# Kernel optimization log

Measured on AMD Instinct MI355X. Metric: run time of the kernel, lower is better.

The kernel has to match this reference:

```python
import jax, jax.numpy as jnp
import numpy as np

N, S, E, H = 8, 1024, 1024, 16
DK = E // H

def setup_inputs() -> dict:
    key = jax.random.key(0)
    ks = jax.random.split(key, 10)
    s = 1.0 / np.sqrt(E)
    x = jax.random.normal(ks[0], (N, S, E), dtype=jnp.float32)
    attn_mask = jax.random.randint(ks[1], (N, S, S), 0, 2) == 1
    Wq = jax.random.normal(ks[2], (E, E), dtype=jnp.float32) * s
    Wk = jax.random.normal(ks[3], (E, E), dtype=jnp.float32) * s
    Wv = jax.random.normal(ks[4], (E, E), dtype=jnp.float32) * s
    Wo = jax.random.normal(ks[5], (E, E), dtype=jnp.float32) * s
    bq = jax.random.normal(ks[6], (E,), dtype=jnp.float32) * s
    bk = jax.random.normal(ks[7], (E,), dtype=jnp.float32) * s
    bv = jax.random.normal(ks[8], (E,), dtype=jnp.float32) * s
    bo = jax.random.normal(ks[9], (E,), dtype=jnp.float32) * s
    return {"x": x, "attn_mask": attn_mask, "Wq": Wq, "bq": bq, "Wk": Wk, "bk": bk,
            "Wv": Wv, "bv": bv, "Wo": Wo, "bo": bo}

def reference(x, attn_mask, Wq, bq, Wk, bk, Wv, bv, Wo, bo):
    n, s, e = x.shape
    # projections, split into heads: (N, H, S, DK)
    q = (x @ Wq + bq).reshape(n, s, H, DK).transpose(0, 2, 1, 3)
    k = (x @ Wk + bk).reshape(n, s, H, DK).transpose(0, 2, 1, 3)
    v = (x @ Wv + bv).reshape(n, s, H, DK).transpose(0, 2, 1, 3)
    logits = jnp.einsum("nhqd,nhkd->nhqk", q, k) / np.sqrt(DK).astype(np.float32)
    # mask==True positions are suppressed (masked_fill with -1e9)
    logits = jnp.where(attn_mask[:, None, :, :], jnp.float32(-1e9), logits)
    attn = jax.nn.softmax(logits, axis=-1)  # exp(log_softmax) == softmax
    o = jnp.einsum("nhqk,nhkd->nhqd", attn, v)
    o = o.transpose(0, 2, 1, 3).reshape(n, s, e)
    return o @ Wo + bo
```

## Files before the change

kernel.cpp:

```cpp
#include <hip/hip_runtime.h>
#include <hip/hip_bf16.h>

typedef unsigned short u16;
typedef unsigned int   u32;
typedef unsigned long long u64;

#define SEQ 1024
#define EMB 1024
#define NH  16
#define DKH 64

#define QSCALE 0.18033688f

typedef __attribute__((ext_vector_type(8))) short short8;
typedef __attribute__((ext_vector_type(4))) float floatx4;

__device__ __forceinline__ float b2f(u16 u) {
  return __uint_as_float(((u32)u) << 16);
}
__device__ __forceinline__ u16 f2b(float f) {
  u32 u = __float_as_uint(f);
  u32 r = u + 0x7fffu + ((u >> 16) & 1u);
  return (u16)(r >> 16);
}

__device__ __forceinline__ void glds16(const u16* g, u16* l) {
  __builtin_amdgcn_global_load_lds(
      (const __attribute__((address_space(1))) u32*)g,
      (__attribute__((address_space(3))) u32*)l, 16, 0, 0);
}

__global__ __launch_bounds__(256) void probe_inputs(const u32* __restrict__ A,
                                                    const u32* __restrict__ B,
                                                    int* __restrict__ flags) {
  __shared__ int mA, mB, mBig, xB16;
  if (threadIdx.x == 0) { mA = 0; mB = 0; mBig = 0; xB16 = 0; }
  __syncthreads();
  int la = 0, lb = 0;
  for (int i = threadIdx.x; i < 4096; i += 256) {
    if ((A[i] & 0xFEFEFEFEu) == 0) la++;
    if ((B[i] & 0xFEFEFEFEu) == 0) lb++;
  }
  atomicAdd(&mA, la); atomicAdd(&mB, lb);
  __syncthreads();
  const int xIsB = (mA > mB) ? 1 : 0;
  const u32* X = xIsB ? B : A;
  const u32* M = xIsB ? A : B;
  int big = 0, cnt = 0;
  for (int i = threadIdx.x; i < 4096; i += 256)
    if (M[i] > 1u) big = 1;
  for (int i = threadIdx.x; i < 2048; i += 256) {
    u16 v = (u16)(X[i] & 0xffffu);
    int e = (v >> 7) & 0xFF;
    if (e >= 110 && e <= 135) cnt++;
  }
  if (big) atomicOr(&mBig, 1);
  atomicAdd(&xB16, cnt);
  __syncthreads();
  if (threadIdx.x == 0) {
    flags[0] = xIsB;
    flags[1] = (xB16 > 1500) ? 1 : 0;
    flags[2] = mBig;
  }
}

__global__ __launch_bounds__(256) void preprocess(
    const void* __restrict__ bigA, const void* __restrict__ bigB,
    const int* __restrict__ flags,
    u16* __restrict__ xb, u32* __restrict__ maskbits,
    const void* __restrict__ w0, const void* __restrict__ w1,
    const void* __restrict__ w2, const void* __restrict__ w3,
    u16* __restrict__ outQKV, u16* __restrict__ outO,
    const void* __restrict__ b0, const void* __restrict__ b1,
    const void* __restrict__ b2, const void* __restrict__ b3,
    float* __restrict__ biasf) {
  __shared__ float tile[32][33];
  const int bidg = blockIdx.x;
  const int t = threadIdx.x;
  const int amode = flags[1];

  if (bidg < 8192) {
    const void* x = flags[0] ? bigB : bigA;
    int i = (bidg * 256 + t) * 4;
    if (amode) {
      *(ushort4*)(xb + i) = *(const ushort4*)((const u16*)x + i);
    } else {
      float4 v = *(const float4*)((const float*)x + i);
      ushort4 o;
      o.x = f2b(v.x); o.y = f2b(v.y); o.z = f2b(v.z); o.w = f2b(v.w);
      *(ushort4*)(xb + i) = o;
    }
  } else if (bidg < 9216) {
    const void* mask = flags[0] ? bigA : bigB;
    const int mbyte = flags[2];
    const int lane = t & 63, wv = t >> 6;
    const u64 base0 = (u64)(bidg - 8192) * 8192;
#pragma unroll 4
    for (int k = 0; k < 32; k++) {
      u64 idx = base0 + k * 256 + t;
      int v;
      if (mbyte) v = ((const unsigned char*)mask)[idx] == 0;
      else       v = ((const u32*)mask)[idx] == 0;
      u64 b = __ballot(v);
      if (lane == 0) {
        u64 wbase = (base0 + k * 256 + wv * 64) >> 5;
        maskbits[wbase]     = (u32)b;
        maskbits[wbase + 1] = (u32)(b >> 32);
      }
    }
  } else if (bidg < 13312) {
    const int idx = bidg - 9216;
    const int z = idx >> 10;
    const int byi = (idx & 1023) >> 5;
    const int bxi = idx & 31;
    const void* in = (z == 0) ? w0 : (z == 1) ? w1 : (z == 2) ? w2 : w3;
    u16* out = (z < 3) ? (outQKV + (u64)z * EMB * EMB) : outO;
    const float scale = (z == 0) ? QSCALE : 1.0f;
    const int tx = t & 31;
    const int ty = t >> 5;
    const int bx = bxi * 32, by = byi * 32;
    if (amode) {
      const u16* inb = (const u16*)in;
#pragma unroll
      for (int r = ty; r < 32; r += 8)
        tile[r][tx] = b2f(inb[(u64)(by + r) * EMB + bx + tx]);
    } else {
      const float* inf = (const float*)in;
#pragma unroll
      for (int r = ty; r < 32; r += 8)
        tile[r][tx] = inf[(u64)(by + r) * EMB + bx + tx];
    }
    __syncthreads();
#pragma unroll
    for (int r = ty; r < 32; r += 8)
      out[(u64)(bx + r) * EMB + by + tx] = f2b(tile[tx][r] * scale);
  } else {
    const int widx = bidg - 13312;
    const void* ptrs[4] = {b0, b1, b2, b3};
    const void* p = ptrs[widx];
    const float scale = (widx == 0) ? QSCALE : 1.0f;
    for (int i = t; i < 1024; i += 256) {
      float v = amode ? b2f(((const u16*)p)[i]) : ((const float*)p)[i];
      biasf[widx * 1024 + i] = v * scale;
    }
  }
}


template <int OUTMODE>
__device__ __forceinline__ void gemm_core(
    const u16* __restrict__ X, const u16* __restrict__ Wt,
    const float* __restrict__ bias,
    u16* __restrict__ Qg, u16* __restrict__ Kg, u16* __restrict__ Vt,
    float* __restrict__ outf, int row0) {
  __shared__ __align__(16) u16 lds[2][(256 + 128) * 64];
  const int t = threadIdx.x;
  const int lane = t & 63;
  const int w = t >> 6;
  const int wr = w >> 1, wc = w & 1;
  const int l15 = lane & 15, l4 = lane >> 4;

  const int nwg = gridDim.x * gridDim.y;
  const int bid0 = blockIdx.y * gridDim.x + blockIdx.x;
  const int cpx = nwg >> 3;
  const int swz = (bid0 & 7) * cpx + (bid0 >> 3);
  const int bM = (swz % gridDim.x) * 256;
  const int bN = (swz / gridDim.x) * 128;

  const int r7 = l15 & 7;
  const int cA = (l4 ^ r7) << 3;
  const int cB = (l4 ^ r7 ^ 4) << 3;

  floatx4 acc[4][4];
#pragma unroll
  for (int i = 0; i < 4; i++)
#pragma unroll
    for (int j = 0; j < 4; j++)
      acc[i][j] = (floatx4){0.f, 0.f, 0.f, 0.f};

  const int srow = w * 8 + (lane >> 3);
  const int schk = ((lane & 7) ^ (lane >> 3)) << 3;
  const u16* Ap = X + (u64)(row0 + bM + srow) * EMB + schk;
  const u16* Bp = Wt + (u64)(bN + srow) * EMB + schk;
  u16* Ad0 = &lds[0][w * 512];
  u16* Bd0 = &lds[0][16384 + w * 512];
  u16* Ad1 = &lds[1][w * 512];
  u16* Bd1 = &lds[1][16384 + w * 512];

  auto stage = [&](u16* Ad, u16* Bd, int k0) {
    glds16(Ap + k0, Ad);
    glds16(Ap + k0 + 64 * EMB, Ad + 4096);
    glds16(Ap + k0 + 128 * EMB, Ad + 8192);
    glds16(Ap + k0 + 192 * EMB, Ad + 12288);
    glds16(Bp + k0, Bd);
    glds16(Bp + k0 + 64 * EMB, Bd + 4096);
  };

  auto compute = [&](const u16* __restrict__ Ab, const u16* __restrict__ Bb) {
    short8 af[2][2], bfr[4][2];
#pragma unroll
    for (int n = 0; n < 4; n++) {
      const int gr = (wc * 64 + n * 16 + l15) * 64;
      bfr[n][0] = *(const short8*)(&Bb[gr + cA]);
      bfr[n][1] = *(const short8*)(&Bb[gr + cB]);
    }
#pragma unroll
    for (int mh = 0; mh < 2; mh++) {
      short8 af2[2][2];
#pragma unroll
      for (int m = 0; m < 2; m++) {
        const int fr = (wr * 64 + mh * 32 + m * 16 + l15) * 64;
        af2[m][0] = *(const short8*)(&Ab[fr + cA]);
        af2[m][1] = *(const short8*)(&Ab[fr + cB]);
      }
      __builtin_amdgcn_s_setprio(1);
#pragma unroll
      for (int m = 0; m < 2; m++)
#pragma unroll
        for (int n = 0; n < 4; n++) {
          acc[mh * 2 + m][n] = __builtin_amdgcn_mfma_f32_16x16x32_bf16(
              af2[m][0], bfr[n][0], acc[mh * 2 + m][n], 0, 0, 0);
          acc[mh * 2 + m][n] = __builtin_amdgcn_mfma_f32_16x16x32_bf16(
              af2[m][1], bfr[n][1], acc[mh * 2 + m][n], 0, 0, 0);
        }
      __builtin_amdgcn_s_setprio(0);
      (void)af[0][0];
    }
  };

  stage(Ad0, Bd0, 0);
  for (int k0 = 0; k0 < EMB; k0 += 128) {
    stage(Ad1, Bd1, k0 + 64);
    asm volatile("s_waitcnt vmcnt(6)" ::: "memory");
    asm volatile("s_barrier" ::: "memory");
    compute(&lds[0][0], &lds[0][16384]);
    asm volatile("s_barrier" ::: "memory");
    if (k0 + 128 < EMB) {
      stage(Ad0, Bd0, k0 + 128);
      asm volatile("s_waitcnt vmcnt(6)" ::: "memory");
    } else {
      asm volatile("s_waitcnt vmcnt(0)" ::: "memory");
    }
    asm volatile("s_barrier" ::: "memory");
    compute(&lds[1][0], &lds[1][16384]);
    asm volatile("s_barrier" ::: "memory");
  }

  if (OUTMODE == 0) {
    const int sec = bN >> 10;
    if (sec < 2) {
      u16* outp = (sec == 0) ? Qg : Kg;
#pragma unroll
      for (int n = 0; n < 4; n++) {
        int col = bN + wc * 64 + n * 16 + l15;
        float bv = bias[col];
        int colh = col & 1023;
        int h = colh >> 6, d = colh & 63;
#pragma unroll
        for (int mt = 0; mt < 4; mt++) {
#pragma unroll
          for (int r = 0; r < 4; r++) {
            int row = bM + wr * 64 + mt * 16 + l4 * 4 + r;
            float v = acc[mt][n][r] + bv;
            int nb = row >> 10, s = row & 1023;
            outp[((u64)((nb * NH + h) * SEQ + s)) * DKH + d] = f2b(v);
          }
        }
      }
    } else {
      u16* ldt = &lds[0][0];
#pragma unroll
      for (int n = 0; n < 4; n++) {
        const int dl = wc * 64 + n * 16 + l15;
        const float bv = bias[bN + dl];
#pragma unroll
        for (int mt = 0; mt < 4; mt++) {
          const int sb = wr * 64 + mt * 16 + l4 * 4;
          const int sp = sb ^ ((dl & 7) << 3);
          u32 w0 = (u32)f2b(acc[mt][n][0] + bv) |
                   ((u32)f2b(acc[mt][n][1] + bv) << 16);
          u32 w1 = (u32)f2b(acc[mt][n][2] + bv) |
                   ((u32)f2b(acc[mt][n][3] + bv) << 16);
          *(u32*)(&ldt[dl * 256 + sp])     = w0;
          *(u32*)(&ldt[dl * 256 + sp + 2]) = w1;
        }
      }
      __syncthreads();
      const int d  = t >> 2;
      const int sq = (t & 3) * 64;
      const int arow = row0 + bM;
      const int nb = arow >> 10, s0 = arow & 1023;
      const int h = ((bN & 1023) >> 6) + (d >> 6);
      u16* vout = Vt + (u64)(nb * NH + h) * SEQ * DKH +
                  (u64)(d & 63) * SEQ + s0 + sq;
#pragma unroll
      for (int c = 0; c < 8; c++) {
        const int sc = sq + c * 8;
        const int scs = sc ^ ((d & 7) << 3);
        *(uint4*)(vout + c * 8) = *(const uint4*)(&ldt[d * 256 + scs]);
      }
    }
  } else {
#pragma unroll
    for (int n = 0; n < 4; n++) {
      int col = bN + wc * 64 + n * 16 + l15;
      float bv = bias[col];
#pragma unroll
      for (int mt = 0; mt < 4; mt++) {
#pragma unroll
        for (int r = 0; r < 4; r++) {
          int row = bM + wr * 64 + mt * 16 + l4 * 4 + r;
          outf[(u64)row * EMB + col] = acc[mt][n][r] + bv;
        }
      }
    }
  }
}

__global__ __launch_bounds__(512, 2) void gemm_qkv(
    const u16* __restrict__ X, const u16* __restrict__ Wt,
    const float* __restrict__ bias,
    u16* __restrict__ Qg, u16* __restrict__ Kg, u16* __restrict__ Vt,
    int row0) {
  gemm_core<0>(X, Wt, bias, Qg, Kg, Vt, nullptr, row0);
}

__global__ __launch_bounds__(512, 2) void gemm_out(
    const u16* __restrict__ X, const u16* __restrict__ Wt,
    const float* __restrict__ bias, float* __restrict__ out) {
  gemm_core<1>(X, Wt, bias, nullptr, nullptr, nullptr, out, 0);
}

__global__ __launch_bounds__(512, 4) void attn_mfma(
    const u16* __restrict__ Q, const u16* __restrict__ K,
    const u16* __restrict__ Vt, const u32* __restrict__ maskbits,
    int b0, u16* __restrict__ ctx) {
  __shared__ __align__(16) u16 Ks[2][64 * 64];
  __shared__ __align__(16) u16 Vs[64 * 64];
  __shared__ __align__(16) u16 Ps[256 * 64];

  const int t = threadIdx.x;
  const int lane = t & 63, w = t >> 6;
  const int l15 = lane & 15, l4 = lane >> 4;
  const int bid = blockIdx.x;
  const int h = bid & 15;
  const int qt = (bid >> 4) & 3;
  const int n = bid >> 6;
  const int nh = n * NH + h;
  const int q0 = qt * 256;
  const u64 hoff = (u64)nh * SEQ * DKH;

  const int r7 = l15 & 7;
  const int cA = (l4 ^ r7) << 3;
  const int cB = (l4 ^ r7 ^ 4) << 3;

  const int rt = w * 8 + (lane >> 3);
  const int chk = ((lane & 7) ^ (lane >> 3)) << 3;
  const u16* Kp = K + hoff + (u64)rt * DKH + chk;
  const u16* Vp = Vt + hoff + (u64)rt * SEQ + chk;
  const int ldsO = w * 512;

  short8 qf[2][2];
  {
    const u16* qpA = Q + hoff + (u64)(q0 + w * 32 + l15) * DKH + l4 * 8;
    qf[0][0] = *(const short8*)(qpA);
    qf[0][1] = *(const short8*)(qpA + 32);
    const u16* qpB = qpA + 16 * DKH;
    qf[1][0] = *(const short8*)(qpB);
    qf[1][1] = *(const short8*)(qpB + 32);
  }

  short8 ones;
#pragma unroll
  for (int e = 0; e < 8; e++) ones[e] = (short)0x3F80;

  floatx4 o[2][4];
#pragma unroll
  for (int s = 0; s < 2; s++)
#pragma unroll
    for (int j = 0; j < 4; j++) o[s][j] = (floatx4){0.f, 0.f, 0.f, 0.f};
  floatx4 osum[2];
  osum[0] = (floatx4){0.f, 0.f, 0.f, 0.f};
  osum[1] = (floatx4){0.f, 0.f, 0.f, 0.f};

  const u64 mrow0 = ((u64)((b0 + n) * SEQ + q0 + w * 32 + l15)) * 32;
  const u64 mrow1 = mrow0 + 16 * 32;
  const int pq0 = w * 32 + l15;
  const int pq1 = pq0 + 16;
  const int pc0 = (l4 * 4) ^ (r7 << 3);

  glds16(Kp, &Ks[0][ldsO]);
  glds16(Vp, &Vs[ldsO]);
  __syncthreads();

  int cur = 0;
  for (int kc = 0; kc < SEQ; kc += 64) {
    if (kc > 0) glds16(Vp + kc, &Vs[ldsO]);
    const int havek = (kc + 64 < SEQ);
    if (havek) glds16(Kp + (kc + 64) * DKH, &Ks[cur ^ 1][ldsO]);

    const u64 mb0 = *(const u64*)(maskbits + mrow0 + (kc >> 5));
    const u64 mb1 = *(const u64*)(maskbits + mrow1 + (kc >> 5));
    const u16* Kc = &Ks[cur][0];

    __builtin_amdgcn_s_setprio(1);
#pragma unroll
    for (int j = 0; j < 4; j++) {
      const int rb = (j * 16 + l15) * 64;
      short8 kb0 = *(const short8*)(&Kc[rb + cA]);
      short8 kb1 = *(const short8*)(&Kc[rb + cB]);
      floatx4 s0 = (floatx4){0.f, 0.f, 0.f, 0.f};
      floatx4 s1 = (floatx4){0.f, 0.f, 0.f, 0.f};
      s0 = __builtin_amdgcn_mfma_f32_16x16x32_bf16(kb0, qf[0][0], s0, 0, 0, 0);
      s0 = __builtin_amdgcn_mfma_f32_16x16x32_bf16(kb1, qf[0][1], s0, 0, 0, 0);
      s1 = __builtin_amdgcn_mfma_f32_16x16x32_bf16(kb0, qf[1][0], s1, 0, 0, 0);
      s1 = __builtin_amdgcn_mfma_f32_16x16x32_bf16(kb1, qf[1][1], s1, 0, 0, 0);

      const u32 mj0 = (u32)(mb0 >> (j * 16 + l4 * 4));
      const u32 mj1 = (u32)(mb1 >> (j * 16 + l4 * 4));
      float p00 = __uint_as_float(
          __float_as_uint(__builtin_amdgcn_exp2f(s0[0])) &
          (u32)__builtin_amdgcn_sbfe(mj0, 0, 1));
      float p01 = __uint_as_float(
          __float_as_uint(__builtin_amdgcn_exp2f(s0[1])) &
          (u32)__builtin_amdgcn_sbfe(mj0, 1, 1));
      float p02 = __uint_as_float(
          __float_as_uint(__builtin_amdgcn_exp2f(s0[2])) &
          (u32)__builtin_amdgcn_sbfe(mj0, 2, 1));
      float p03 = __uint_as_float(
          __float_as_uint(__builtin_amdgcn_exp2f(s0[3])) &
          (u32)__builtin_amdgcn_sbfe(mj0, 3, 1));
      float p10 = __uint_as_float(
          __float_as_uint(__builtin_amdgcn_exp2f(s1[0])) &
          (u32)__builtin_amdgcn_sbfe(mj1, 0, 1));
      float p11 = __uint_as_float(
          __float_as_uint(__builtin_amdgcn_exp2f(s1[1])) &
          (u32)__builtin_amdgcn_sbfe(mj1, 1, 1));
      float p12 = __uint_as_float(
          __float_as_uint(__builtin_amdgcn_exp2f(s1[2])) &
          (u32)__builtin_amdgcn_sbfe(mj1, 2, 1));
      float p13 = __uint_as_float(
          __float_as_uint(__builtin_amdgcn_exp2f(s1[3])) &
          (u32)__builtin_amdgcn_sbfe(mj1, 3, 1));

      uint2 pk0, pk1;
      asm("v_cvt_pk_bf16_f32 %0, %1, %2" : "=v"(pk0.x) : "v"(p00), "v"(p01));
      asm("v_cvt_pk_bf16_f32 %0, %1, %2" : "=v"(pk0.y) : "v"(p02), "v"(p03));
      asm("v_cvt_pk_bf16_f32 %0, %1, %2" : "=v"(pk1.x) : "v"(p10), "v"(p11));
      asm("v_cvt_pk_bf16_f32 %0, %1, %2" : "=v"(pk1.y) : "v"(p12), "v"(p13));
      const int pcol = (j * 16) ^ pc0;
      *(uint2*)(&Ps[pq0 * 64 + pcol]) = pk0;
      *(uint2*)(&Ps[pq1 * 64 + pcol]) = pk1;
    }

    if (havek) asm volatile("s_waitcnt vmcnt(1)" ::: "memory");
    else       asm volatile("s_waitcnt vmcnt(0)" ::: "memory");
    __builtin_amdgcn_s_barrier();

    short8 pa[2][2];
    pa[0][0] = *(const short8*)(&Ps[pq0 * 64 + cA]);
    pa[0][1] = *(const short8*)(&Ps[pq0 * 64 + cB]);
    pa[1][0] = *(const short8*)(&Ps[pq1 * 64 + cA]);
    pa[1][1] = *(const short8*)(&Ps[pq1 * 64 + cB]);
#pragma unroll
    for (int j = 0; j < 4; j++) {
      const int rb = (j * 16 + l15) * 64;
      short8 vb0 = *(const short8*)(&Vs[rb + cA]);
      short8 vb1 = *(const short8*)(&Vs[rb + cB]);
      o[0][j] = __builtin_amdgcn_mfma_f32_16x16x32_bf16(pa[0][0], vb0, o[0][j], 0, 0, 0);
      o[0][j] = __builtin_amdgcn_mfma_f32_16x16x32_bf16(pa[0][1], vb1, o[0][j], 0, 0, 0);
      o[1][j] = __builtin_amdgcn_mfma_f32_16x16x32_bf16(pa[1][0], vb0, o[1][j], 0, 0, 0);
      o[1][j] = __builtin_amdgcn_mfma_f32_16x16x32_bf16(pa[1][1], vb1, o[1][j], 0, 0, 0);
    }
    osum[0] = __builtin_amdgcn_mfma_f32_16x16x32_bf16(pa[0][0], ones, osum[0], 0, 0, 0);
    osum[0] = __builtin_amdgcn_mfma_f32_16x16x32_bf16(pa[0][1], ones, osum[0], 0, 0, 0);
    osum[1] = __builtin_amdgcn_mfma_f32_16x16x32_bf16(pa[1][0], ones, osum[1], 0, 0, 0);
    osum[1] = __builtin_amdgcn_mfma_f32_16x16x32_bf16(pa[1][1], ones, osum[1], 0, 0, 0);
    __builtin_amdgcn_s_setprio(0);

    __syncthreads();
    cur ^= 1;
  }

#pragma unroll
  for (int s = 0; s < 2; s++) {
#pragma unroll
    for (int r = 0; r < 4; r++) {
      float invr = 1.0f / fmaxf(osum[s][r], 1e-30f);
      int q = q0 + w * 32 + s * 16 + l4 * 4 + r;
      u64 base = ((u64)(n * SEQ + q)) * EMB + h * DKH + l15;
#pragma unroll
      for (int j = 0; j < 4; j++)
        ctx[base + j * 16] = f2b(o[s][j][r] * invr);
    }
  }
}

extern "C" void kernel_launch(void* const* d_in, const int* in_sizes, int n_in,
                              void* d_out, int out_size, void* d_ws, size_t ws_size,
                              hipStream_t stream) {
  int bigI[2] = {0, 1}, wI[4] = {2, 4, 6, 8}, bI[4] = {3, 5, 7, 9};
  int nb = 0, nw = 0, nbi = 0;
  for (int i = 0; i < n_in; i++) {
    if (in_sizes[i] == 8388608) { if (nb < 2) bigI[nb++] = i; }
    else if (in_sizes[i] == 1048576) { if (nw < 4) wI[nw++] = i; }
    else if (in_sizes[i] == 1024) { if (nbi < 4) bI[nbi++] = i; }
  }
  int oq = 0, ok = 1, ov = 2, oo = 3;
  if (nb == 2 && bigI[0] == 4 && bigI[1] == 9) { oq = 2; ok = 0; ov = 3; oo = 1; }

  const void* bigA = d_in[bigI[0]];
  const void* bigB = d_in[bigI[1]];
  const void* Wq = d_in[wI[oq]];
  const void* Wk = d_in[wI[ok]];
  const void* Wv = d_in[wI[ov]];
  const void* Wo = d_in[wI[oo]];
  const void* bq = d_in[bI[oq]];
  const void* bk = d_in[bI[ok]];
  const void* bv = d_in[bI[ov]];
  const void* bo = d_in[bI[oo]];

  char* ws = (char*)d_ws;
  u16* WtQKV = (u16*)ws;
  u16* WtO   = (u16*)(ws + (6ull << 20));
  float* biasf = (float*)(ws + (8ull << 20));
  int* flags = (int*)(ws + (8ull << 20) + 16384);
  u32* maskbits = (u32*)(ws + (8ull << 20) + 65536);
  u16* xb = (u16*)(ws + (10ull << 20));
  char* grp = ws + (26ull << 20);

  int G = 1;
  for (int g = 8; g >= 1; g >>= 1) {
    if (ws_size >= (26ull << 20) + (u64)g * (8ull << 20)) { G = g; break; }
  }
  const u64 gsz = (u64)G * (2ull << 20);
  u16* Qg = (u16*)grp;
  u16* Kg = (u16*)(grp + gsz);
  u16* ctx = (u16*)(grp + 2 * gsz);
  u16* Vt = (u16*)(grp + 3 * gsz);

  dim3 tb(256);

  probe_inputs<<<dim3(1), tb, 0, stream>>>((const u32*)bigA, (const u32*)bigB, flags);

  preprocess<<<dim3(13316), tb, 0, stream>>>(
      bigA, bigB, flags, xb, maskbits,
      Wq, Wk, Wv, Wo, WtQKV, WtO,
      bq, bk, bv, bo, biasf);

  for (int b0 = 0; b0 < 8; b0 += G) {
    int row0 = b0 * 1024;
    gemm_qkv<<<dim3(4 * G, 24), dim3(512), 0, stream>>>(xb, WtQKV, biasf, Qg, Kg, Vt, row0);

    attn_mfma<<<dim3(G * 16 * 4), dim3(512), 0, stream>>>(Qg, Kg, Vt, maskbits, b0, ctx);

    gemm_out<<<dim3(4 * G, 8), dim3(512), 0, stream>>>(ctx, WtO, biasf + 3072,
                                                       (float*)d_out + (u64)row0 * EMB);
  }
}
```

Baseline: 320.8 us.

## Stage Q/K GEMM epilogue through LDS for coalesced stores; drop block swizzle

After: 291.2 us. 1.1x faster.

```diff
diff --git a/kernel.cpp b/kernel.cpp
--- a/kernel.cpp
+++ b/kernel.cpp
@@ -159,14 +159,7 @@
   const int w = t >> 6;
   const int wr = w >> 1, wc = w & 1;
   const int l15 = lane & 15, l4 = lane >> 4;
-
-  const int nwg = gridDim.x * gridDim.y;
-  const int bid0 = blockIdx.y * gridDim.x + blockIdx.x;
-  const int cpx = nwg >> 3;
-  const int swz = (bid0 & 7) * cpx + (bid0 >> 3);
-  const int bM = (swz % gridDim.x) * 256;
-  const int bN = (swz / gridDim.x) * 128;
-
+  const int bM = blockIdx.x * 256, bN = blockIdx.y * 128;
   const int r7 = l15 & 7;
   const int cA = (l4 ^ r7) << 3;
   const int cB = (l4 ^ r7 ^ 4) << 3;
@@ -197,7 +190,7 @@
   };
 
   auto compute = [&](const u16* __restrict__ Ab, const u16* __restrict__ Bb) {
-    short8 af[2][2], bfr[4][2];
+    short8 bfr[4][2];
 #pragma unroll
     for (int n = 0; n < 4; n++) {
       const int gr = (wc * 64 + n * 16 + l15) * 64;
@@ -224,7 +217,6 @@
               af2[m][1], bfr[n][1], acc[mh * 2 + m][n], 0, 0, 0);
         }
       __builtin_amdgcn_s_setprio(0);
-      (void)af[0][0];
     }
   };
 
@@ -248,23 +240,35 @@
 
   if (OUTMODE == 0) {
     const int sec = bN >> 10;
+    const int nb = bM >> 10;
     if (sec < 2) {
       u16* outp = (sec == 0) ? Qg : Kg;
+      u16* ldt = &lds[0][0];
 #pragma unroll
       for (int n = 0; n < 4; n++) {
-        int col = bN + wc * 64 + n * 16 + l15;
-        float bv = bias[col];
-        int colh = col & 1023;
-        int h = colh >> 6, d = colh & 63;
+        const int cl = wc * 64 + n * 16 + l15;
+        const float bv = bias[bN + cl];
 #pragma unroll
         for (int mt = 0; mt < 4; mt++) {
 #pragma unroll
           for (int r = 0; r < 4; r++) {
-            int row = bM + wr * 64 + mt * 16 + l4 * 4 + r;
-            float v = acc[mt][n][r] + bv;
-            int nb = row >> 10, s = row & 1023;
-            outp[((u64)((nb * NH + h) * SEQ + s)) * DKH + d] = f2b(v);
+            const int rl = wr * 64 + mt * 16 + l4 * 4 + r;
+            ldt[rl * 136 + cl] = f2b(acc[mt][n][r] + bv);
           }
+        }
+      }
+      __syncthreads();
+      const int h0 = (bN & 1023) >> 6;
+      const int s0 = bM & 1023;
+#pragma unroll
+      for (int hh = 0; hh < 2; hh++) {
+        u16* basep = outp + ((u64)(nb * NH + h0 + hh) * SEQ + s0) * DKH;
+#pragma unroll
+        for (int kk = 0; kk < 4; kk++) {
+          const int ci = t + 512 * kk;
+          const int s = ci >> 3, d0 = (ci & 7) * 8;
+          *(uint4*)(basep + s * 64 + d0) =
+              *(const uint4*)(&ldt[s * 136 + hh * 64 + d0]);
         }
       }
     } else {
@@ -288,8 +292,7 @@
       __syncthreads();
       const int d  = t >> 2;
       const int sq = (t & 3) * 64;
-      const int arow = row0 + bM;
-      const int nb = arow >> 10, s0 = arow & 1023;
+      const int s0 = bM & 1023;
       const int h = ((bN & 1023) >> 6) + (d >> 6);
       u16* vout = Vt + (u64)(nb * NH + h) * SEQ * DKH +
                   (u64)(d & 63) * SEQ + s0 + sq;
```
